# Kernel optimization log

Hardware: AMD Instinct MI355X
Metric: run time of the kernel (lower is better)

## Reference

```python
import jax, jax.numpy as jnp
import numpy as np

EMB = 1024
NH = 16
DH = EMB // NH
SCALE = np.sqrt(EMB).astype(np.float32)  # module scales by sqrt(emb_dim), not sqrt(d_head)


def setup_inputs() -> dict:
    key = jax.random.key(0)
    ks = jax.random.split(key, 9)
    s = 1.0 / np.sqrt(EMB)
    return {
        "a": jax.random.normal(ks[0], (4, 2048, EMB), jnp.float32),
        "Wq": jax.random.normal(ks[1], (EMB, EMB), jnp.float32) * s,
        "bq": jnp.zeros((EMB,), jnp.float32),
        "Wk": jax.random.normal(ks[2], (EMB, EMB), jnp.float32) * s,
        "bk": jnp.zeros((EMB,), jnp.float32),
        "Wv": jax.random.normal(ks[3], (EMB, EMB), jnp.float32) * s,
        "bv": jnp.zeros((EMB,), jnp.float32),
        "Wo": jax.random.normal(ks[4], (EMB, EMB), jnp.float32) * s,
        "bo": jnp.zeros((EMB,), jnp.float32),
    }


def reference(a, Wq, bq, Wk, bk, Wv, bv, Wo, bo):
    N, S, _ = a.shape
    # Q/K/V projections (self-attention: b is None -> b = a)
    Q = (a @ Wq + bq).reshape(N, S, NH, DH).transpose(0, 2, 1, 3)  # [N,H,A,D]
    K = (a @ Wk + bk).reshape(N, S, NH, DH).transpose(0, 2, 1, 3)  # [N,H,B,D]
    V = (a @ Wv + bv).reshape(N, S, NH, DH).transpose(0, 2, 1, 3)  # [N,H,B,D]
    score = jnp.einsum('nhad,nhbd->nhab', Q, K) / SCALE
    score = jax.nn.softmax(score, axis=-1)
    out = jnp.einsum('nhab,nhbd->nhad', score, V)                  # [N,H,A,D]
    out = out.transpose(0, 2, 1, 3).reshape(N, S, EMB)
    return out @ Wo + bo
```

## Files before the change

kernel.cpp:

```cpp
#include <hip/hip_runtime.h>
#include <hip/hip_bf16.h>
#include <stdint.h>

typedef __attribute__((ext_vector_type(8))) short short8v;
typedef __attribute__((ext_vector_type(4))) float float4v;

#define GLDS16(gp, lp) __builtin_amdgcn_global_load_lds( \
    (const __attribute__((address_space(1))) void*)(gp),  \
    (__attribute__((address_space(3))) void*)(lp), 16, 0, 0)

#if __has_builtin(__builtin_amdgcn_exp2f)
#define EXP2(x) __builtin_amdgcn_exp2f(x)
#else
#define EXP2(x) exp2f(x)
#endif

#define LOG2E 1.4426950408889634f

__global__ __launch_bounds__(256) void cast_a_kernel(
    const float* __restrict__ src, __hip_bfloat16* __restrict__ dst, int n4) {
  int i = blockIdx.x * blockDim.x + threadIdx.x;
  if (i < n4) {
    float4 v = ((const float4*)src)[i];
    union { __hip_bfloat16 h[4]; ushort4 u; } p;
    p.h[0] = __float2bfloat16(v.x);
    p.h[1] = __float2bfloat16(v.y);
    p.h[2] = __float2bfloat16(v.z);
    p.h[3] = __float2bfloat16(v.w);
    ((ushort4*)dst)[i] = p.u;
  }
}

__global__ __launch_bounds__(256) void transpose4_kernel(
    const float* __restrict__ Wq, const float* __restrict__ Wk,
    const float* __restrict__ Wv, const float* __restrict__ Wo,
    __hip_bfloat16* __restrict__ Wcat, __hip_bfloat16* __restrict__ WoT) {
  __shared__ float t[32][33];
  const int z = blockIdx.z;
  const float* W = (z == 0) ? Wq : (z == 1) ? Wk : (z == 2) ? Wv : Wo;
  __hip_bfloat16* dst = (z < 3) ? (Wcat + (size_t)z * 1048576) : WoT;
  int tx = threadIdx.x & 31, ty = threadIdx.x >> 5;
  int r0 = blockIdx.y * 32, c0 = blockIdx.x * 32;
#pragma unroll
  for (int i = 0; i < 4; ++i) {
    int r = ty + i * 8;
    t[r][tx] = W[(size_t)(r0 + r) * 1024 + c0 + tx];
  }
  __syncthreads();
#pragma unroll
  for (int i = 0; i < 4; ++i) {
    int r = ty + i * 8;
    dst[(size_t)(c0 + r) * 1024 + r0 + tx] = __float2bfloat16(t[tx][r]);
  }
}

__global__ __launch_bounds__(512, 2) void gemm_qkv8_kernel(
    const __hip_bfloat16* __restrict__ A, const __hip_bfloat16* __restrict__ BT,
    const float* __restrict__ bq, const float* __restrict__ bk,
    const float* __restrict__ bv, __hip_bfloat16* __restrict__ Qh,
    __hip_bfloat16* __restrict__ Kh, __hip_bfloat16* __restrict__ Vt) {
  __shared__ char lds[131072];
  const int tid = threadIdx.x;
  const int l = tid & 63, w = tid >> 6;
  const int g = l >> 4, cc = l & 15;
  const int wm = w >> 2, wn = w & 3;
  const int sw = (cc & 7) << 4;
  const int bid = blockIdx.x;
  const int nbid = (bid & 7) * 48 + (bid >> 3);
  const int tm = nbid / 12, tn = nbid % 12;
  const int m0 = tm * 256, n0 = tn * 256;

  const int scol = ((tid & 7) * 16) ^ (((tid >> 3) & 7) << 4);
  const char* pA = (const char*)A + (size_t)(m0 + (tid >> 3)) * 2048 + scol;
  const char* pB = (const char*)BT + (size_t)(n0 + (tid >> 3)) * 2048 + scol;
  char* ldsT = lds + tid * 16;

#define STGH(pG, base, half, kt) {                                            \
    GLDS16((pG) + ((half) * 128) * 2048 + (kt) * 128,                         \
           ldsT + (base) + (half) * 16384);                                   \
    GLDS16((pG) + ((half) * 128 + 64) * 2048 + (kt) * 128,                    \
           ldsT + (base) + (half) * 16384 + 8192);                            \
  }

  short8v af[4][2], bf[4][2];
#define DSA(base, fmb)                                                        \
  _Pragma("unroll") for (int i = 0; i < 4; ++i)                               \
  _Pragma("unroll") for (int kk = 0; kk < 2; ++kk)                            \
    af[i][kk] = *(const short8v*)(lds + (base) +                              \
        (((wm * 128 + ((fmb) + i) * 16 + cc) * 128 + kk * 64 + g * 16) ^ sw));
#define DSB(base, np)                                                        \
  _Pragma("unroll") for (int ii = 0; ii < 2; ++ii)                            \
  _Pragma("unroll") for (int kk = 0; kk < 2; ++kk)                            \
    bf[(np) * 2 + ii][kk] = *(const short8v*)(lds + (base) +                  \
        (((wn * 64 + ((np) * 2 + ii) * 16 + cc) * 128 + kk * 64 + g * 16) ^ sw));

  float4v acc[8][4];
#pragma unroll
  for (int m = 0; m < 8; ++m)
#pragma unroll
    for (int n = 0; n < 4; ++n) acc[m][n] = (float4v){0.f, 0.f, 0.f, 0.f};

#define MM(fmb, np)                                                           \
  __builtin_amdgcn_s_setprio(1);                                              \
  _Pragma("unroll") for (int i = 0; i < 4; ++i)                               \
  _Pragma("unroll") for (int ii = 0; ii < 2; ++ii)                            \
  _Pragma("unroll") for (int kk = 0; kk < 2; ++kk)                            \
    acc[(fmb) + i][(np) * 2 + ii] = __builtin_amdgcn_mfma_f32_16x16x32_bf16(  \
        af[i][kk], bf[(np) * 2 + ii][kk], acc[(fmb) + i][(np) * 2 + ii], 0, 0, 0); \
  __builtin_amdgcn_s_setprio(0);

#define BAR() __builtin_amdgcn_s_barrier()
#define WAIT4() asm volatile("s_waitcnt vmcnt(4)" ::: "memory")

  STGH(pB, 65536, 0, 0); STGH(pB, 65536, 1, 0);
  STGH(pA, 0, 0, 0);     STGH(pA, 0, 1, 0);
  STGH(pB, 98304, 0, 1); STGH(pB, 98304, 1, 1);
  WAIT4();
  BAR();

  for (int j = 0; j < 8; ++j) {
    const int vv = 2 * j + 1;
    const int u2 = (j < 7) ? 2 * j + 2 : 15;
    const int v2 = (j < 7) ? 2 * j + 3 : 15;
    DSA(0, 0); DSB(65536, 0);
    STGH(pA, 32768, 0, vv);
    BAR(); MM(0, 0); BAR();
    DSB(65536, 1);
    STGH(pA, 32768, 1, vv);
    BAR(); MM(0, 1); BAR();
    DSA(0, 4);
    STGH(pB, 65536, 0, u2);
    BAR(); MM(4, 0); BAR();
    STGH(pB, 65536, 1, u2);
    WAIT4();
    BAR(); MM(4, 1); BAR();
    DSA(32768, 0); DSB(98304, 0);
    STGH(pA, 0, 0, u2);
    BAR(); MM(0, 0); BAR();
    DSB(98304, 1);
    STGH(pA, 0, 1, u2);
    BAR(); MM(0, 1); BAR();
    DSA(32768, 4);
    STGH(pB, 98304, 0, v2);
    BAR(); MM(4, 0); BAR();
    STGH(pB, 98304, 1, v2);
    WAIT4();
    BAR(); MM(4, 1); BAR();
  }
#undef STGH
#undef DSA
#undef DSB
#undef MM
#undef BAR
#undef WAIT4

  const int sec = n0 >> 10;
  if (sec < 2) {
    __hip_bfloat16* out = sec == 0 ? Qh : Kh;
    const float* bias = sec == 0 ? bq : bk;
    const float scale = sec == 0 ? (LOG2E / 32.f) : 1.f;
#pragma unroll
    for (int m = 0; m < 8; ++m) {
#pragma unroll
      for (int n = 0; n < 4; ++n) {
        int colc = (n0 + wn * 64 + n * 16 + cc) & 1023;
        float b = bias[colc];
        int h = colc >> 6, d = colc & 63;
#pragma unroll
        for (int r = 0; r < 4; ++r) {
          int grow = m0 + wm * 128 + m * 16 + g * 4 + r;
          int nb = grow >> 11, s = grow & 2047;
          out[((size_t)(nb * 16 + h) * 2048 + s) * 64 + d] =
              __float2bfloat16((acc[m][n][r] + b) * scale);
        }
      }
    }
  } else {
#pragma unroll
    for (int m = 0; m < 8; ++m) {
      int grow0 = m0 + wm * 128 + m * 16 + g * 4;
      int nb = grow0 >> 11, key0 = grow0 & 2047;
      int kp0 = (key0 & ~31) | ((key0 & 12) << 1) | (((key0 >> 4) & 1) << 2);
#pragma unroll
      for (int n = 0; n < 4; ++n) {
        int colc = (n0 + wn * 64 + n * 16 + cc) & 1023;
        float b = bv[colc];
        int h = colc >> 6, d = colc & 63;
        union { __hip_bfloat16 h4[4]; uint2 u; } pk;
#pragma unroll
        for (int r = 0; r < 4; ++r) pk.h4[r] = __float2bfloat16(acc[m][n][r] + b);
        *(uint2*)&Vt[((size_t)((nb * 16 + h) * 64 + d)) * 2048 + kp0] = pk.u;
      }
    }
  }
}

__global__ __launch_bounds__(256, 2) void gemm_o_kernel(
    const __hip_bfloat16* __restrict__ A, const __hip_bfloat16* __restrict__ BT,
    const float* __restrict__ bias, float* __restrict__ C) {
  __shared__ char lds[32768];
  const int tid = threadIdx.x;
  const int l = tid & 63, w = tid >> 6;
  const int g = l >> 4, cc = l & 15;
  const int bid = blockIdx.x;
  const int nbid = (bid & 7) * 64 + (bid >> 3);
  const int m0 = (nbid & 63) * 128, n0 = (nbid >> 6) * 128;
  const int wm = w >> 1, wn = w & 1;

  float4v acc[4][4];
#pragma unroll
  for (int m = 0; m < 4; ++m)
#pragma unroll
    for (int n = 0; n < 4; ++n) acc[m][n] = (float4v){0.f, 0.f, 0.f, 0.f};

  for (int kt = 0; kt < 16; ++kt) {
#pragma unroll
    for (int j = 0; j < 4; ++j) {
      int ci = (w * 4 + j) * 64 + l;
      int row = ci >> 3, ko = (ci & 7) * 16;
      GLDS16((const char*)A + (size_t)(m0 + row) * 2048 + kt * 128 + ko,
             lds + ci * 16);
      GLDS16((const char*)BT + (size_t)(n0 + row) * 2048 + kt * 128 + ko,
             lds + 16384 + ci * 16);
    }
    __syncthreads();
#pragma unroll
    for (int h = 0; h < 2; ++h) {
      short8v af[4], bf[4];
#pragma unroll
      for (int m = 0; m < 4; ++m)
        af[m] = *(const short8v*)(lds + (wm * 64 + m * 16 + cc) * 128 + h * 64 + g * 16);
#pragma unroll
      for (int n = 0; n < 4; ++n)
        bf[n] = *(const short8v*)(lds + 16384 + (wn * 64 + n * 16 + cc) * 128 + h * 64 + g * 16);
#pragma unroll
      for (int m = 0; m < 4; ++m)
#pragma unroll
        for (int n = 0; n < 4; ++n)
          acc[m][n] = __builtin_amdgcn_mfma_f32_16x16x32_bf16(af[m], bf[n], acc[m][n], 0, 0, 0);
    }
    __syncthreads();
  }

#pragma unroll
  for (int m = 0; m < 4; ++m) {
    int row = m0 + wm * 64 + m * 16 + g * 4;
#pragma unroll
    for (int n = 0; n < 4; ++n) {
      int col = n0 + wn * 64 + n * 16 + cc;
      float b = bias[col];
#pragma unroll
      for (int r = 0; r < 4; ++r)
        C[(size_t)(row + r) * 1024 + col] = acc[m][n][r] + b;
    }
  }
}

__global__ __launch_bounds__(512, 4) void attn_kernel(
    const __hip_bfloat16* __restrict__ Q,
    const __hip_bfloat16* __restrict__ K,
    const __hip_bfloat16* __restrict__ VT,
    __hip_bfloat16* __restrict__ AO) {
  __shared__ char sK[3][8192];
  __shared__ char sV[4][8192];
  const int tid = threadIdx.x;
  const int l = tid & 63, w = tid >> 6;
  const int g = l >> 4, cc = l & 15;
  const int bid = blockIdx.x;
  const int nbid = (bid & 7) * 64 + (bid >> 3);
  const int bx = nbid & 7, nh = nbid >> 3;
  const int q0 = bx * 256 + w * 32;
  const char* Kb = (const char*)(K + (size_t)nh * 131072);
  const char* Vb = (const char*)(VT + (size_t)nh * 131072);
  const __hip_bfloat16* Qb = Q + (size_t)nh * 131072;

  short8v qf[2][2];
#pragma unroll
  for (int qg = 0; qg < 2; ++qg)
#pragma unroll
    for (int dh = 0; dh < 2; ++dh)
      qf[qg][dh] = *(const short8v*)(Qb + (size_t)(q0 + qg * 16 + cc) * 64 + dh * 32 + g * 8);

  int koff[4][2], voff[4][2];
#pragma unroll
  for (int kg = 0; kg < 4; ++kg)
#pragma unroll
    for (int dh = 0; dh < 2; ++dh) {
      int row = kg * 16 + cc;
      koff[kg][dh] = (row * 128 + dh * 64 + g * 16) ^ ((row & 7) << 4);
    }
#pragma unroll
  for (int f = 0; f < 4; ++f)
#pragma unroll
    for (int hh = 0; hh < 2; ++hh) {
      int d = f * 16 + cc;
      voff[f][hh] = (d * 128 + hh * 64 + g * 16) ^ ((d & 7) << 4);
    }
  const int ss = tid * 16;
  const int sr = ss >> 7;
  const int soff = (ss & 127) ^ ((sr & 7) << 4);
  const int stKo = sr * 128 + soff;
  const int stVo = sr * 4096 + soff;

  const short8v fone = {16256, 16256, 16256, 16256, 16256, 16256, 16256, 16256};

  float lr[2] = {0.f, 0.f};
  float4v oacc[2][4];
#pragma unroll
  for (int qg = 0; qg < 2; ++qg)
#pragma unroll
    for (int f = 0; f < 4; ++f) oacc[qg][f] = (float4v){0.f, 0.f, 0.f, 0.f};

#define STAGE(kb, vb, ktv)                                                    \
  {                                                                           \
    GLDS16(Kb + (size_t)(ktv) * 8192 + stKo, (kb) + ss);                      \
    GLDS16(Vb + (size_t)(ktv) * 128 + stVo, (vb) + ss);                       \
  }

#define QKBLK(KSRC, SV)                                                       \
  {                                                                           \
    short8v kf_[4][2];                                                        \
    _Pragma("unroll") for (int kg = 0; kg < 4; ++kg)                          \
    _Pragma("unroll") for (int dh = 0; dh < 2; ++dh)                          \
      kf_[kg][dh] = *(const short8v*)((KSRC) + koff[kg][dh]);                 \
    _Pragma("unroll") for (int qg = 0; qg < 2; ++qg)                          \
    _Pragma("unroll") for (int kg = 0; kg < 4; ++kg) {                        \
      float4v z_ = (float4v){0.f, 0.f, 0.f, 0.f};                             \
      z_ = __builtin_amdgcn_mfma_f32_16x16x32_bf16(kf_[kg][0], qf[qg][0], z_, 0, 0, 0); \
      (SV)[qg][kg] = __builtin_amdgcn_mfma_f32_16x16x32_bf16(kf_[kg][1], qf[qg][1], z_, 0, 0, 0); \
    }                                                                         \
  }

#define PVBLK(VSRC)                                                           \
  {                                                                           \
    _Pragma("unroll") for (int f = 0; f < 4; ++f)                             \
    _Pragma("unroll") for (int hh = 0; hh < 2; ++hh) {                        \
      short8v vk_ = *(const short8v*)((VSRC) + voff[f][hh]);                  \
      _Pragma("unroll") for (int qg = 0; qg < 2; ++qg)                        \
        oacc[qg][f] = __builtin_amdgcn_mfma_f32_16x16x32_bf16(vk_, pfP[qg][hh], oacc[qg][f], 0, 0, 0); \
    }                                                                         \
    _Pragma("unroll") for (int qg = 0; qg < 2; ++qg) {                        \
      float4v t_ = (float4v){0.f, 0.f, 0.f, 0.f};                             \
      t_ = __builtin_amdgcn_mfma_f32_16x16x32_bf16(fone, pfP[qg][0], t_, 0, 0, 0); \
      t_ = __builtin_amdgcn_mfma_f32_16x16x32_bf16(fone, pfP[qg][1], t_, 0, 0, 0); \
      lr[qg] += t_[0];                                                        \
    }                                                                         \
  }

#define SMBLK(SV)                                                             \
  {                                                                           \
    _Pragma("unroll") for (int qg = 0; qg < 2; ++qg) {                        \
      _Pragma("unroll") for (int kg = 0; kg < 4; ++kg)                        \
      _Pragma("unroll") for (int r = 0; r < 4; ++r)                           \
        (SV)[qg][kg][r] = EXP2((SV)[qg][kg][r]);                              \
      _Pragma("unroll") for (int hh = 0; hh < 2; ++hh) {                      \
        union { __hip_bfloat16 h[8]; short8v v8; } pk_;                       \
        _Pragma("unroll") for (int j = 0; j < 4; ++j) {                       \
          pk_.h[j]     = __float2bfloat16((SV)[qg][2 * hh][j]);               \
          pk_.h[4 + j] = __float2bfloat16((SV)[qg][2 * hh + 1][j]);           \
        }                                                                     \
        pfP[qg][hh] = pk_.v8;                                                 \
      }                                                                       \
    }                                                                         \
  }

  short8v pfP[2][2];
  char *kc = sK[0], *kn = sK[1], *ks = sK[2];
  char *vp = sV[0], *vc = sV[1], *vn = sV[2], *vs = sV[3];

  STAGE(sK[0], sV[0], 0);
  STAGE(sK[1], sV[1], 1);
  asm volatile("s_waitcnt vmcnt(2)" ::: "memory");
  __builtin_amdgcn_s_barrier();
  STAGE(sK[2], sV[2], 2);
  {
    float4v sv[2][4];
    QKBLK(sK[0], sv);
    SMBLK(sv);
  }
  kc = sK[1]; kn = sK[2]; ks = sK[0];
  vp = sV[0]; vc = sV[1]; vn = sV[2]; vs = sV[3];

  for (int t = 1; t <= 31; ++t) {
    if (t < 31) {
      asm volatile("s_waitcnt vmcnt(2)" ::: "memory");
    } else {
      asm volatile("s_waitcnt vmcnt(0)" ::: "memory");
    }
    __builtin_amdgcn_s_barrier();
    if (t <= 29) STAGE(ks, vs, t + 2);

    float4v sv[2][4];
    QKBLK(kc, sv);
    PVBLK(vp);
    SMBLK(sv);

    char* tt;
    tt = kc; kc = kn; kn = ks; ks = tt;
    tt = vp; vp = vc; vc = vn; vn = vs; vs = tt;
  }
  PVBLK(vp);
#undef STAGE
#undef QKBLK
#undef PVBLK
#undef SMBLK

  int nb = nh >> 4, h = nh & 15;
#pragma unroll
  for (int qg = 0; qg < 2; ++qg) {
    float inv = 1.f / lr[qg];
    int qrow = q0 + qg * 16 + cc;
#pragma unroll
    for (int f = 0; f < 4; ++f)
#pragma unroll
      for (int r = 0; r < 4; ++r) {
        int d = f * 16 + g * 4 + r;
        AO[(size_t)(nb * 2048 + qrow) * 1024 + h * 64 + d] =
            __float2bfloat16(oacc[qg][f][r] * inv);
      }
  }
}

extern "C" void kernel_launch(void* const* d_in, const int* in_sizes, int n_in,
                              void* d_out, int out_size, void* d_ws, size_t ws_size,
                              hipStream_t stream) {
  const float* a  = (const float*)d_in[0];
  const float* Wq = (const float*)d_in[1];
  const float* bq = (const float*)d_in[2];
  const float* Wk = (const float*)d_in[3];
  const float* bk = (const float*)d_in[4];
  const float* Wv = (const float*)d_in[5];
  const float* bv = (const float*)d_in[6];
  const float* Wo = (const float*)d_in[7];
  const float* bo = (const float*)d_in[8];

  char* ws = (char*)d_ws;
  __hip_bfloat16* aB   = (__hip_bfloat16*)(ws);
  __hip_bfloat16* Wcat = (__hip_bfloat16*)(ws + (16ull << 20));
  __hip_bfloat16* WoT  = (__hip_bfloat16*)(ws + (22ull << 20));
  __hip_bfloat16* Qh   = (__hip_bfloat16*)(ws + (24ull << 20));
  __hip_bfloat16* Kh   = (__hip_bfloat16*)(ws + (40ull << 20));
  __hip_bfloat16* Vt   = (__hip_bfloat16*)(ws + (56ull << 20));
  __hip_bfloat16* AOb  = (__hip_bfloat16*)(ws + (72ull << 20));

  cast_a_kernel<<<8192, 256, 0, stream>>>(a, aB, 8192 * 1024 / 4);
  dim3 tg(32, 32, 4);
  transpose4_kernel<<<tg, 256, 0, stream>>>(Wq, Wk, Wv, Wo, Wcat, WoT);

  gemm_qkv8_kernel<<<384, 512, 0, stream>>>(aB, Wcat, bq, bk, bv, Qh, Kh, Vt);

  attn_kernel<<<512, 512, 0, stream>>>(Qh, Kh, Vt, AOb);

  gemm_o_kernel<<<512, 256, 0, stream>>>(AOb, WoT, bo, (float*)d_out);
}
```

Before: 184.9 us.

## Load K/V tiles directly into registers in attention, dropping LDS staging

The attention kernel no longer stages K and V tiles through shared memory with async global-to-LDS copies and barriers. Each wave now loads its K and V fragments straight from global memory into registers, double-buffering K two tiles ahead and V one tile ahead. Blocks shrink to 256 threads, with each wave handling 64 query rows instead of 32. This removes barriers and LDS traffic, but every wave now re-reads the same K/V from global memory or L2 and register pressure rises.

New measurement: 227.6 us. 1.23x slower.

```diff
diff --git a/kernel.cpp b/kernel.cpp
--- a/kernel.cpp
+++ b/kernel.cpp
@@ -256,158 +256,104 @@
   }
 }
 
-__global__ __launch_bounds__(512, 4) void attn_kernel(
+__global__ __launch_bounds__(256, 2) void attn_kernel(
     const __hip_bfloat16* __restrict__ Q,
     const __hip_bfloat16* __restrict__ K,
     const __hip_bfloat16* __restrict__ VT,
     __hip_bfloat16* __restrict__ AO) {
-  __shared__ char sK[3][8192];
-  __shared__ char sV[4][8192];
   const int tid = threadIdx.x;
   const int l = tid & 63, w = tid >> 6;
   const int g = l >> 4, cc = l & 15;
   const int bid = blockIdx.x;
   const int nbid = (bid & 7) * 64 + (bid >> 3);
   const int bx = nbid & 7, nh = nbid >> 3;
-  const int q0 = bx * 256 + w * 32;
+  const int q0 = bx * 256 + w * 64;
   const char* Kb = (const char*)(K + (size_t)nh * 131072);
   const char* Vb = (const char*)(VT + (size_t)nh * 131072);
   const __hip_bfloat16* Qb = Q + (size_t)nh * 131072;
 
-  short8v qf[2][2];
-#pragma unroll
-  for (int qg = 0; qg < 2; ++qg)
+  short8v qf[4][2];
+#pragma unroll
+  for (int qg = 0; qg < 4; ++qg)
 #pragma unroll
     for (int dh = 0; dh < 2; ++dh)
       qf[qg][dh] = *(const short8v*)(Qb + (size_t)(q0 + qg * 16 + cc) * 64 + dh * 32 + g * 8);
 
-  int koff[4][2], voff[4][2];
-#pragma unroll
-  for (int kg = 0; kg < 4; ++kg)
-#pragma unroll
-    for (int dh = 0; dh < 2; ++dh) {
-      int row = kg * 16 + cc;
-      koff[kg][dh] = (row * 128 + dh * 64 + g * 16) ^ ((row & 7) << 4);
-    }
-#pragma unroll
-  for (int f = 0; f < 4; ++f)
-#pragma unroll
-    for (int hh = 0; hh < 2; ++hh) {
-      int d = f * 16 + cc;
-      voff[f][hh] = (d * 128 + hh * 64 + g * 16) ^ ((d & 7) << 4);
-    }
-  const int ss = tid * 16;
-  const int sr = ss >> 7;
-  const int soff = (ss & 127) ^ ((sr & 7) << 4);
-  const int stKo = sr * 128 + soff;
-  const int stVo = sr * 4096 + soff;
+  const char* Kl = Kb + cc * 128 + g * 16;
+  const char* Vl = Vb + (size_t)cc * 4096 + g * 16;
 
   const short8v fone = {16256, 16256, 16256, 16256, 16256, 16256, 16256, 16256};
 
-  float lr[2] = {0.f, 0.f};
-  float4v oacc[2][4];
-#pragma unroll
-  for (int qg = 0; qg < 2; ++qg)
+  float lr[4] = {0.f, 0.f, 0.f, 0.f};
+  float4v oacc[4][4];
+#pragma unroll
+  for (int qg = 0; qg < 4; ++qg)
 #pragma unroll
     for (int f = 0; f < 4; ++f) oacc[qg][f] = (float4v){0.f, 0.f, 0.f, 0.f};
 
-#define STAGE(kb, vb, ktv)                                                    \
+  short8v ka[4][2], kb2[4][2], vk[4][2];
+
+#define LDK(DST, T)                                                           \
+  _Pragma("unroll") for (int kg = 0; kg < 4; ++kg)                            \
+  _Pragma("unroll") for (int dh = 0; dh < 2; ++dh)                            \
+    DST[kg][dh] = *(const short8v*)(Kl + (size_t)(T) * 8192 + kg * 2048 + dh * 64);
+
+#define LDV(T)                                                                \
+  _Pragma("unroll") for (int f = 0; f < 4; ++f)                               \
+  _Pragma("unroll") for (int hh = 0; hh < 2; ++hh)                            \
+    vk[f][hh] = *(const short8v*)(Vl + (size_t)(f) * 65536 + (size_t)(T) * 128 + hh * 64);
+
+#define BODY(T, KC, DOV, DOK)                                                 \
   {                                                                           \
-    GLDS16(Kb + (size_t)(ktv) * 8192 + stKo, (kb) + ss);                      \
-    GLDS16(Vb + (size_t)(ktv) * 128 + stVo, (vb) + ss);                       \
-  }
-
-#define QKBLK(KSRC, SV)                                                       \
-  {                                                                           \
-    short8v kf_[4][2];                                                        \
-    _Pragma("unroll") for (int kg = 0; kg < 4; ++kg)                          \
-    _Pragma("unroll") for (int dh = 0; dh < 2; ++dh)                          \
-      kf_[kg][dh] = *(const short8v*)((KSRC) + koff[kg][dh]);                 \
-    _Pragma("unroll") for (int qg = 0; qg < 2; ++qg)                          \
-    _Pragma("unroll") for (int kg = 0; kg < 4; ++kg) {                        \
-      float4v z_ = (float4v){0.f, 0.f, 0.f, 0.f};                             \
-      z_ = __builtin_amdgcn_mfma_f32_16x16x32_bf16(kf_[kg][0], qf[qg][0], z_, 0, 0, 0); \
-      (SV)[qg][kg] = __builtin_amdgcn_mfma_f32_16x16x32_bf16(kf_[kg][1], qf[qg][1], z_, 0, 0, 0); \
-    }                                                                         \
-  }
-
-#define PVBLK(VSRC)                                                           \
-  {                                                                           \
-    _Pragma("unroll") for (int f = 0; f < 4; ++f)                             \
-    _Pragma("unroll") for (int hh = 0; hh < 2; ++hh) {                        \
-      short8v vk_ = *(const short8v*)((VSRC) + voff[f][hh]);                  \
-      _Pragma("unroll") for (int qg = 0; qg < 2; ++qg)                        \
-        oacc[qg][f] = __builtin_amdgcn_mfma_f32_16x16x32_bf16(vk_, pfP[qg][hh], oacc[qg][f], 0, 0, 0); \
-    }                                                                         \
-    _Pragma("unroll") for (int qg = 0; qg < 2; ++qg) {                        \
+    _Pragma("unroll") for (int qg = 0; qg < 4; ++qg) {                        \
+      float4v sv[4];                                                          \
+      _Pragma("unroll") for (int kg = 0; kg < 4; ++kg) {                      \
+        float4v z_ = (float4v){0.f, 0.f, 0.f, 0.f};                           \
+        z_ = __builtin_amdgcn_mfma_f32_16x16x32_bf16(KC[kg][0], qf[qg][0], z_, 0, 0, 0); \
+        sv[kg] = __builtin_amdgcn_mfma_f32_16x16x32_bf16(KC[kg][1], qf[qg][1], z_, 0, 0, 0); \
+      }                                                                       \
+      _Pragma("unroll") for (int kg = 0; kg < 4; ++kg)                        \
+      _Pragma("unroll") for (int r = 0; r < 4; ++r) sv[kg][r] = EXP2(sv[kg][r]); \
+      short8v pf[2];                                                          \
+      _Pragma("unroll") for (int hh = 0; hh < 2; ++hh) {                      \
+        union { __hip_bfloat16 h[8]; short8v v8; } pk_;                       \
+        _Pragma("unroll") for (int jj = 0; jj < 4; ++jj) {                    \
+          pk_.h[jj]     = __float2bfloat16(sv[2 * hh][jj]);                   \
+          pk_.h[4 + jj] = __float2bfloat16(sv[2 * hh + 1][jj]);               \
+        }                                                                     \
+        pf[hh] = pk_.v8;                                                      \
+      }                                                                       \
+      _Pragma("unroll") for (int f = 0; f < 4; ++f)                           \
+      _Pragma("unroll") for (int hh = 0; hh < 2; ++hh)                        \
+        oacc[qg][f] = __builtin_amdgcn_mfma_f32_16x16x32_bf16(vk[f][hh], pf[hh], oacc[qg][f], 0, 0, 0); \
       float4v t_ = (float4v){0.f, 0.f, 0.f, 0.f};                             \
-      t_ = __builtin_amdgcn_mfma_f32_16x16x32_bf16(fone, pfP[qg][0], t_, 0, 0, 0); \
-      t_ = __builtin_amdgcn_mfma_f32_16x16x32_bf16(fone, pfP[qg][1], t_, 0, 0, 0); \
+      t_ = __builtin_amdgcn_mfma_f32_16x16x32_bf16(fone, pf[0], t_, 0, 0, 0); \
+      t_ = __builtin_amdgcn_mfma_f32_16x16x32_bf16(fone, pf[1], t_, 0, 0, 0); \
       lr[qg] += t_[0];                                                        \
     }                                                                         \
-  }
-
-#define SMBLK(SV)                                                             \
-  {                                                                           \
-    _Pragma("unroll") for (int qg = 0; qg < 2; ++qg) {                        \
-      _Pragma("unroll") for (int kg = 0; kg < 4; ++kg)                        \
-      _Pragma("unroll") for (int r = 0; r < 4; ++r)                           \
-        (SV)[qg][kg][r] = EXP2((SV)[qg][kg][r]);                              \
-      _Pragma("unroll") for (int hh = 0; hh < 2; ++hh) {                      \
-        union { __hip_bfloat16 h[8]; short8v v8; } pk_;                       \
-        _Pragma("unroll") for (int j = 0; j < 4; ++j) {                       \
-          pk_.h[j]     = __float2bfloat16((SV)[qg][2 * hh][j]);               \
-          pk_.h[4 + j] = __float2bfloat16((SV)[qg][2 * hh + 1][j]);           \
-        }                                                                     \
-        pfP[qg][hh] = pk_.v8;                                                 \
-      }                                                                       \
-    }                                                                         \
-  }
-
-  short8v pfP[2][2];
-  char *kc = sK[0], *kn = sK[1], *ks = sK[2];
-  char *vp = sV[0], *vc = sV[1], *vn = sV[2], *vs = sV[3];
-
-  STAGE(sK[0], sV[0], 0);
-  STAGE(sK[1], sV[1], 1);
-  asm volatile("s_waitcnt vmcnt(2)" ::: "memory");
-  __builtin_amdgcn_s_barrier();
-  STAGE(sK[2], sV[2], 2);
-  {
-    float4v sv[2][4];
-    QKBLK(sK[0], sv);
-    SMBLK(sv);
-  }
-  kc = sK[1]; kn = sK[2]; ks = sK[0];
-  vp = sV[0]; vc = sV[1]; vn = sV[2]; vs = sV[3];
-
-  for (int t = 1; t <= 31; ++t) {
-    if (t < 31) {
-      asm volatile("s_waitcnt vmcnt(2)" ::: "memory");
-    } else {
-      asm volatile("s_waitcnt vmcnt(0)" ::: "memory");
-    }
-    __builtin_amdgcn_s_barrier();
-    if (t <= 29) STAGE(ks, vs, t + 2);
-
-    float4v sv[2][4];
-    QKBLK(kc, sv);
-    PVBLK(vp);
-    SMBLK(sv);
-
-    char* tt;
-    tt = kc; kc = kn; kn = ks; ks = tt;
-    tt = vp; vp = vc; vc = vn; vn = vs; vs = tt;
-  }
-  PVBLK(vp);
-#undef STAGE
-#undef QKBLK
-#undef PVBLK
-#undef SMBLK
+    if (DOV) { LDV((T) + 1); }                                                \
+    if (DOK) { LDK(KC, (T) + 2); }                                            \
+  }
+
+  LDK(ka, 0);
+  LDV(0);
+  LDK(kb2, 1);
+
+#pragma unroll 1
+  for (int j = 0; j < 15; ++j) {
+    const int t0 = 2 * j;
+    BODY(t0, ka, 1, 1);
+    BODY(t0 + 1, kb2, 1, 1);
+  }
+  BODY(30, ka, 1, 0);
+  BODY(31, kb2, 0, 0);
+#undef LDK
+#undef LDV
+#undef BODY
 
   int nb = nh >> 4, h = nh & 15;
 #pragma unroll
-  for (int qg = 0; qg < 2; ++qg) {
+  for (int qg = 0; qg < 4; ++qg) {
     float inv = 1.f / lr[qg];
     int qrow = q0 + qg * 16 + cc;
 #pragma unroll
@@ -449,7 +395,7 @@
 
   gemm_qkv8_kernel<<<384, 512, 0, stream>>>(aB, Wcat, bq, bk, bv, Qh, Kh, Vt);
 
-  attn_kernel<<<512, 512, 0, stream>>>(Qh, Kh, Vt, AOb);
+  attn_kernel<<<512, 256, 0, stream>>>(Qh, Kh, Vt, AOb);
 
   gemm_o_kernel<<<512, 256, 0, stream>>>(AOb, WoT, bo, (float*)d_out);
 }
```

## Replace software-pipelined attention loop with double-buffered two-tile steps

Applied to the files above, without the earlier changes.

Restructures the attention inner loop. Before, QK^T of tile t+1 was interleaved with PV of tile t, using a 3-deep K ring and a 4-deep V ring. Now each iteration waits for all loads, stages the next pair of K/V tiles into the other half of a 4-slot buffer, and processes two tiles back to back, each doing QK, exp, pack and PV in sequence. This halves the number of barriers and simplifies register live ranges. The cost is losing the cross-stage overlap between QK and PV MFMAs, and every iteration now waits with vmcnt(0).

After: 178.6 us. 1.04x faster.

```diff
diff --git a/kernel.cpp b/kernel.cpp
--- a/kernel.cpp
+++ b/kernel.cpp
@@ -261,7 +261,7 @@
     const __hip_bfloat16* __restrict__ K,
     const __hip_bfloat16* __restrict__ VT,
     __hip_bfloat16* __restrict__ AO) {
-  __shared__ char sK[3][8192];
+  __shared__ char sK[4][8192];
   __shared__ char sV[4][8192];
   const int tid = threadIdx.x;
   const int l = tid & 63, w = tid >> 6;
@@ -317,93 +317,61 @@
     GLDS16(Vb + (size_t)(ktv) * 128 + stVo, (vb) + ss);                       \
   }
 
-#define QKBLK(KSRC, SV)                                                       \
+#define TILE(KSRC, VSRC)                                                      \
   {                                                                           \
-    short8v kf_[4][2];                                                        \
+    short8v kf[4][2];                                                         \
     _Pragma("unroll") for (int kg = 0; kg < 4; ++kg)                          \
     _Pragma("unroll") for (int dh = 0; dh < 2; ++dh)                          \
-      kf_[kg][dh] = *(const short8v*)((KSRC) + koff[kg][dh]);                 \
-    _Pragma("unroll") for (int qg = 0; qg < 2; ++qg)                          \
-    _Pragma("unroll") for (int kg = 0; kg < 4; ++kg) {                        \
-      float4v z_ = (float4v){0.f, 0.f, 0.f, 0.f};                             \
-      z_ = __builtin_amdgcn_mfma_f32_16x16x32_bf16(kf_[kg][0], qf[qg][0], z_, 0, 0, 0); \
-      (SV)[qg][kg] = __builtin_amdgcn_mfma_f32_16x16x32_bf16(kf_[kg][1], qf[qg][1], z_, 0, 0, 0); \
+      kf[kg][dh] = *(const short8v*)((KSRC) + koff[kg][dh]);                  \
+    short8v pf[2][2];                                                         \
+    _Pragma("unroll") for (int qg = 0; qg < 2; ++qg) {                        \
+      float4v sv[4];                                                          \
+      _Pragma("unroll") for (int kg = 0; kg < 4; ++kg) {                      \
+        float4v z = (float4v){0.f, 0.f, 0.f, 0.f};                            \
+        z = __builtin_amdgcn_mfma_f32_16x16x32_bf16(kf[kg][0], qf[qg][0], z, 0, 0, 0); \
+        sv[kg] = __builtin_amdgcn_mfma_f32_16x16x32_bf16(kf[kg][1], qf[qg][1], z, 0, 0, 0); \
+      }                                                                       \
+      _Pragma("unroll") for (int kg = 0; kg < 4; ++kg)                        \
+      _Pragma("unroll") for (int r = 0; r < 4; ++r) sv[kg][r] = EXP2(sv[kg][r]); \
+      _Pragma("unroll") for (int hh = 0; hh < 2; ++hh) {                      \
+        union { __hip_bfloat16 h[8]; short8v v8; } pk;                        \
+        _Pragma("unroll") for (int jj = 0; jj < 4; ++jj) {                    \
+          pk.h[jj]     = __float2bfloat16(sv[2 * hh][jj]);                    \
+          pk.h[4 + jj] = __float2bfloat16(sv[2 * hh + 1][jj]);                \
+        }                                                                     \
+        pf[qg][hh] = pk.v8;                                                   \
+      }                                                                       \
+      float4v t = (float4v){0.f, 0.f, 0.f, 0.f};                              \
+      t = __builtin_amdgcn_mfma_f32_16x16x32_bf16(fone, pf[qg][0], t, 0, 0, 0); \
+      t = __builtin_amdgcn_mfma_f32_16x16x32_bf16(fone, pf[qg][1], t, 0, 0, 0); \
+      lr[qg] += t[0];                                                         \
     }                                                                         \
-  }
-
-#define PVBLK(VSRC)                                                           \
-  {                                                                           \
     _Pragma("unroll") for (int f = 0; f < 4; ++f)                             \
     _Pragma("unroll") for (int hh = 0; hh < 2; ++hh) {                        \
-      short8v vk_ = *(const short8v*)((VSRC) + voff[f][hh]);                  \
+      short8v vk = *(const short8v*)((VSRC) + voff[f][hh]);                   \
       _Pragma("unroll") for (int qg = 0; qg < 2; ++qg)                        \
-        oacc[qg][f] = __builtin_amdgcn_mfma_f32_16x16x32_bf16(vk_, pfP[qg][hh], oacc[qg][f], 0, 0, 0); \
+        oacc[qg][f] = __builtin_amdgcn_mfma_f32_16x16x32_bf16(vk, pf[qg][hh], oacc[qg][f], 0, 0, 0); \
     }                                                                         \
-    _Pragma("unroll") for (int qg = 0; qg < 2; ++qg) {                        \
-      float4v t_ = (float4v){0.f, 0.f, 0.f, 0.f};                             \
-      t_ = __builtin_amdgcn_mfma_f32_16x16x32_bf16(fone, pfP[qg][0], t_, 0, 0, 0); \
-      t_ = __builtin_amdgcn_mfma_f32_16x16x32_bf16(fone, pfP[qg][1], t_, 0, 0, 0); \
-      lr[qg] += t_[0];                                                        \
-    }                                                                         \
-  }
-
-#define SMBLK(SV)                                                             \
-  {                                                                           \
-    _Pragma("unroll") for (int qg = 0; qg < 2; ++qg) {                        \
-      _Pragma("unroll") for (int kg = 0; kg < 4; ++kg)                        \
-      _Pragma("unroll") for (int r = 0; r < 4; ++r)                           \
-        (SV)[qg][kg][r] = EXP2((SV)[qg][kg][r]);                              \
-      _Pragma("unroll") for (int hh = 0; hh < 2; ++hh) {                      \
-        union { __hip_bfloat16 h[8]; short8v v8; } pk_;                       \
-        _Pragma("unroll") for (int j = 0; j < 4; ++j) {                       \
-          pk_.h[j]     = __float2bfloat16((SV)[qg][2 * hh][j]);               \
-          pk_.h[4 + j] = __float2bfloat16((SV)[qg][2 * hh + 1][j]);           \
-        }                                                                     \
-        pfP[qg][hh] = pk_.v8;                                                 \
-      }                                                                       \
-    }                                                                         \
-  }
-
-  short8v pfP[2][2];
-  char *kc = sK[0], *kn = sK[1], *ks = sK[2];
-  char *vp = sV[0], *vc = sV[1], *vn = sV[2], *vs = sV[3];
+  }
 
   STAGE(sK[0], sV[0], 0);
   STAGE(sK[1], sV[1], 1);
-  asm volatile("s_waitcnt vmcnt(2)" ::: "memory");
-  __builtin_amdgcn_s_barrier();
-  STAGE(sK[2], sV[2], 2);
-  {
-    float4v sv[2][4];
-    QKBLK(sK[0], sv);
-    SMBLK(sv);
-  }
-  kc = sK[1]; kn = sK[2]; ks = sK[0];
-  vp = sV[0]; vc = sV[1]; vn = sV[2]; vs = sV[3];
-
-  for (int t = 1; t <= 31; ++t) {
-    if (t < 31) {
-      asm volatile("s_waitcnt vmcnt(2)" ::: "memory");
-    } else {
-      asm volatile("s_waitcnt vmcnt(0)" ::: "memory");
-    }
+
+#pragma unroll 1
+  for (int j = 0; j < 16; ++j) {
+    asm volatile("s_waitcnt vmcnt(0)" ::: "memory");
     __builtin_amdgcn_s_barrier();
-    if (t <= 29) STAGE(ks, vs, t + 2);
-
-    float4v sv[2][4];
-    QKBLK(kc, sv);
-    PVBLK(vp);
-    SMBLK(sv);
-
-    char* tt;
-    tt = kc; kc = kn; kn = ks; ks = tt;
-    tt = vp; vp = vc; vc = vn; vn = vs; vs = tt;
-  }
-  PVBLK(vp);
+    const int p = (j & 1) << 1;
+    const int s = p ^ 2;
+    if (j < 15) {
+      STAGE(sK[s], sV[s], 2 * j + 2);
+      STAGE(sK[s + 1], sV[s + 1], 2 * j + 3);
+    }
+    TILE(sK[p], sV[p]);
+    TILE(sK[p + 1], sV[p + 1]);
+  }
 #undef STAGE
-#undef QKBLK
-#undef PVBLK
-#undef SMBLK
+#undef TILE
 
   int nb = nh >> 4, h = nh & 15;
 #pragma unroll
```
